# Performance work log

Hardware: AMD Instinct MI355X
Metric: run time of the kernel (lower is better)

Reference implementation:

```python
import jax, jax.numpy as jnp
import numpy as np

B, S, H, NH, DH, F, L = 4, 2048, 512, 8, 64, 2048, 4
ALPHA = 1.0   # config.lag_time_scale_alpha
EPS = 1e-12   # BERT layer_norm_eps
MS_PER_MIN = 60.0 * 1000.0


def setup_inputs() -> dict:
    key = jax.random.key(0)
    ks = jax.random.split(key, 24)
    p = lambda k, shape: (jax.random.normal(k, shape, jnp.float32) * 0.02)
    inp = {
        "query_states": jax.random.normal(ks[0], (B, S, H), jnp.float32),
        "attention_mask": jnp.zeros((B, 1, 1, S), jnp.float32),
        "position_bias": jax.random.normal(ks[1], (1, NH, S, S), jnp.float32) * 0.02,
        "timestamp": jnp.sort(jax.random.randint(ks[2], (B, S), 0, 36_000_000, jnp.int32), axis=-1),
        # stacked per-layer parameters (L leading dim)
        "wq": p(ks[3], (L, H, H)), "bq": jnp.zeros((L, H), jnp.float32),
        "wk": p(ks[4], (L, H, H)), "bk": jnp.zeros((L, H), jnp.float32),
        "wv": p(ks[5], (L, H, H)), "bv": jnp.zeros((L, H), jnp.float32),
        "wo": p(ks[6], (L, H, H)), "bo": jnp.zeros((L, H), jnp.float32),
        "ln1_g": jnp.ones((L, H), jnp.float32), "ln1_b": jnp.zeros((L, H), jnp.float32),
        "wi": p(ks[7], (L, H, F)), "bi": jnp.zeros((L, F), jnp.float32),
        "wo2": p(ks[8], (L, F, H)), "bo2": jnp.zeros((L, H), jnp.float32),
        "ln2_g": jnp.ones((L, H), jnp.float32), "ln2_b": jnp.zeros((L, H), jnp.float32),
    }
    return inp


def _ln(x, g, b):
    m = x.mean(-1, keepdims=True)
    v = ((x - m) ** 2).mean(-1, keepdims=True)
    return (x - m) / jnp.sqrt(v + EPS) * g + b


def reference(query_states, attention_mask, position_bias, timestamp,
              wq, bq, wk, bk, wv, bv, wo, bo, ln1_g, ln1_b,
              wi, bi, wo2, bo2, ln2_g, ln2_b):
    # encoder (is_decoder=False) lag-time scale: (B,1,S,S)
    lag = (timestamp[:, None, :, None] - timestamp[:, None, None, :]).astype(jnp.float32) / MS_PER_MIN
    scale = np.sqrt(DH).astype(np.float32) - ALPHA / (jnp.clip(lag, 0.0) + 1.0) + ALPHA

    x = query_states
    for l in range(L):
        def proj(w, b):
            return (x @ w + b).reshape(B, S, NH, DH).transpose(0, 2, 1, 3)  # (B,NH,S,DH)
        q, k, v = proj(wq[l], bq[l]), proj(wk[l], bk[l]), proj(wv[l], bv[l])
        scores = jnp.einsum('bhqd,bhkd->bhqk', q, k) / scale + position_bias + attention_mask
        probs = jax.nn.softmax(scores, axis=-1)
        ctx = jnp.einsum('bhqk,bhkd->bhqd', probs, v).transpose(0, 2, 1, 3).reshape(B, S, H)
        attn = _ln(ctx @ wo[l] + bo[l] + x, ln1_g[l], ln1_b[l])
        ffn = jax.nn.gelu(attn @ wi[l] + bi[l], approximate=False) @ wo2[l] + bo2[l]
        x = _ln(ffn + attn, ln2_g[l], ln2_b[l])
    return x
```

## Files before the change

kernel.cpp:

```cpp
#include <hip/hip_runtime.h>
#include <stdint.h>

typedef unsigned short u16;
using half8   = __attribute__((ext_vector_type(8))) _Float16;
using half4v  = __attribute__((ext_vector_type(4))) _Float16;
using half2v  = __attribute__((ext_vector_type(2))) _Float16;
using float4v = __attribute__((ext_vector_type(4))) float;

#define L2E 1.4426950408889634f

__device__ inline float4v f4zero() { float4v z = {0.f, 0.f, 0.f, 0.f}; return z; }

__device__ inline u16 f2h(float f) {
  union { _Float16 h; u16 u; } v; v.h = (_Float16)f; return v.u;
}
__device__ inline float h2f(u16 u) {
  union { u16 u; _Float16 h; } v; v.u = u; return (float)v.h;
}

__device__ inline half2v cvtpk(float a, float b) {
  return __builtin_bit_cast(half2v, __builtin_amdgcn_cvt_pkrtz(a, b));
}
__device__ inline _Float16 hexp2_(_Float16 x) {
  _Float16 r;
  asm("v_exp_f16 %0, %1" : "=v"(r) : "v"(x));
  return r;
}
__device__ inline float fdot2f(half2v a, float c) {
#if __has_builtin(__builtin_amdgcn_fdot2)
  typedef __attribute__((ext_vector_type(2))) __fp16 h2r;
  return __builtin_amdgcn_fdot2(__builtin_bit_cast(h2r, a),
                                __builtin_bit_cast(h2r, 0x3C003C00u), c, false);
#else
  return c + (float)a.x + (float)a.y;
#endif
}

__device__ inline void glds16(const u16* g, u16* lds_base, int lane) {
#if __has_builtin(__builtin_amdgcn_global_load_lds)
  (void)lane;
  __builtin_amdgcn_global_load_lds((const __attribute__((address_space(1))) void*)g,
                                   (__attribute__((address_space(3))) void*)lds_base,
                                   16, 0, 0);
#else
  *(uint4*)(lds_base + (size_t)lane * 8) = *(const uint4*)g;
#endif
}

__global__ __launch_bounds__(256) void transpose_cast_kernel(
    const float* __restrict__ in, u16* __restrict__ out, int K, int N, size_t out_ls) {
  __shared__ float tile[32][33];
  const int tx = threadIdx.x & 31, ty = threadIdx.x >> 5;
  in  += (size_t)blockIdx.z * K * N;
  out += (size_t)blockIdx.z * out_ls;
  const int n  = blockIdx.x * 32 + tx;
  const int k0 = blockIdx.y * 32;
#pragma unroll
  for (int j = 0; j < 32; j += 8)
    tile[ty + j][tx] = in[(size_t)(k0 + ty + j) * N + n];
  __syncthreads();
  const int k = k0 + tx;
  const int n0 = blockIdx.x * 32;
#pragma unroll
  for (int j = 0; j < 32; j += 8)
    out[(size_t)(n0 + ty + j) * K + k] = f2h(tile[tx][ty + j]);
}

__global__ __launch_bounds__(256) void cast_kernel(const float* __restrict__ in,
                                                   u16* __restrict__ out) {
  const int i = (blockIdx.x * 256 + threadIdx.x) * 4;
  float4 t = *(const float4*)(in + i);
  ushort4 o;
  o.x = f2h(t.x); o.y = f2h(t.y); o.z = f2h(t.z); o.w = f2h(t.w);
  *(ushort4*)(out + i) = o;
}

__global__ __launch_bounds__(256) void pb_tile_kernel(const float* __restrict__ pb,
                                                      u16* __restrict__ pbT) {
  const int g  = blockIdx.x * 256 + threadIdx.x;
  const int mm = g & 15;
  const int q  = (g >> 4) & 2047;
  const int kbh = g >> 15;
  const int kb = kbh & 31, h = kbh >> 5;
  const float* src = pb + ((size_t)h * 2048 + q) * 2048 + kb * 64 + mm;
  ushort4 o;
  o.x = f2h(src[0]  * L2E);
  o.y = f2h(src[16] * L2E);
  o.z = f2h(src[32] * L2E);
  o.w = f2h(src[48] * L2E);
  *(ushort4*)(pbT + ((size_t)(h * 32 + kb) * 2048 + q) * 64 + mm * 4) = o;
}

__global__ __launch_bounds__(256) void inv_tile_kernel(const int* __restrict__ ts,
                                                       u16* __restrict__ invT) {
  const int g  = blockIdx.x * 256 + threadIdx.x;
  const int mm = g & 15;
  const int q  = (g >> 4) & 2047;
  const int kb = (g >> 15) & 31;
  const int b  = g >> 20;
  const int tq = ts[b * 2048 + q];
  ushort4 o;
  u16* op = (u16*)&o;
#pragma unroll
  for (int nb = 0; nb < 4; nb++) {
    const int k = kb * 64 + nb * 16 + mm;
    const int du = tq - ts[b * 2048 + k];
    const float u = (du > 0) ? (float)du : 0.f;
    op[nb] = f2h(fmaf(u, L2E, 86561.70245333781f) *
                 __builtin_amdgcn_rcpf(fmaf(u, 9.f, 480000.f)));
  }
  *(ushort4*)(invT + ((size_t)(b * 32 + kb) * 2048 + q) * 64 + mm * 4) = o;
}

__global__ __launch_bounds__(256) void maskts_kernel(const float* __restrict__ mask,
                                                     const int* __restrict__ ts,
                                                     float* __restrict__ maskE,
                                                     float* __restrict__ tsf) {
  const int i = blockIdx.x * 256 + threadIdx.x;
  maskE[i] = mask[i] * L2E;
  tsf[i]   = (float)ts[i];
}

template <int BM, int BN, int NN, int KK, int EPI>
__global__ __launch_bounds__(256) void gemm_kernel(
    const u16* __restrict__ A, const u16* __restrict__ Wt,
    const float* __restrict__ b0, const float* __restrict__ b1, const float* __restrict__ b2,
    const u16* __restrict__ resid,
    void* __restrict__ o0, void* __restrict__ o1, void* __restrict__ o2) {
  constexpr int FI = BM / 32;
  constexpr int FJB = BN / 32;
  constexpr int FIW = BM / 32;
  constexpr int FJW = BN / 32;
  constexpr int NT = KK / 64;
  __shared__ __align__(16) u16 smem[2 * BM * 64 + 2 * BN * 64];
  u16* As0 = smem;
  u16* Bs0 = smem + 2 * BM * 64;
  const int tid = threadIdx.x, lane = tid & 63, wv = tid >> 6;
  const int quad = lane >> 4, mm = lane & 15;
  const int m0 = blockIdx.x * BM, n0 = blockIdx.y * BN;
  const int wm = (wv >> 1) * (BM / 2), wn = (wv & 1) * (BN / 2);
  const int srow = tid >> 3, slot = tid & 7;
  const int chunk = slot ^ (srow & 7);
  const u16* Ag = A  + (size_t)(m0 + srow) * KK + chunk * 8;
  const u16* Bg = Wt + (size_t)(n0 + srow) * KK + chunk * 8;
  const int sw = mm & 7;

  float4v acc[FIW][FJW];
#pragma unroll
  for (int i = 0; i < FIW; i++)
#pragma unroll
    for (int j = 0; j < FJW; j++) acc[i][j] = f4zero();

#pragma unroll
  for (int i = 0; i < FI; i++)
    glds16(Ag + (size_t)i * 32 * KK, As0 + (size_t)(wv * 8 + i * 32) * 64, lane);
#pragma unroll
  for (int j = 0; j < FJB; j++)
    glds16(Bg + (size_t)j * 32 * KK, Bs0 + (size_t)(wv * 8 + j * 32) * 64, lane);

  int cur = 0;
#pragma unroll 2
  for (int kt = 0; kt < NT; kt++) {
    __syncthreads();

    if (kt + 1 < NT) {
      const size_t ko = (size_t)(kt + 1) * 64;
#pragma unroll
      for (int i = 0; i < FI; i++)
        glds16(Ag + (size_t)i * 32 * KK + ko,
               As0 + (size_t)(cur ^ 1) * BM * 64 + (size_t)(wv * 8 + i * 32) * 64, lane);
#pragma unroll
      for (int j = 0; j < FJB; j++)
        glds16(Bg + (size_t)j * 32 * KK + ko,
               Bs0 + (size_t)(cur ^ 1) * BN * 64 + (size_t)(wv * 8 + j * 32) * 64, lane);
    }

    const u16* Ac = As0 + (size_t)cur * BM * 64;
    const u16* Bc = Bs0 + (size_t)cur * BN * 64;
#pragma unroll
    for (int ks = 0; ks < 2; ks++) {
      half8 a[FIW], b[FJW];
#pragma unroll
      for (int i = 0; i < FIW; i++)
        a[i] = *(const half8*)(Ac + (size_t)(wm + i * 16 + mm) * 64 + (size_t)((ks * 4 + quad) ^ sw) * 8);
#pragma unroll
      for (int j = 0; j < FJW; j++)
        b[j] = *(const half8*)(Bc + (size_t)(wn + j * 16 + mm) * 64 + (size_t)((ks * 4 + quad) ^ sw) * 8);
#pragma unroll
      for (int i = 0; i < FIW; i++)
#pragma unroll
        for (int j = 0; j < FJW; j++)
          acc[i][j] = __builtin_amdgcn_mfma_f32_16x16x32_f16(a[i], b[j], acc[i][j], 0, 0, 0);
    }
    cur ^= 1;
  }

#pragma unroll
  for (int j = 0; j < FJW; j++) {
    const int gn = n0 + wn + j * 16 + mm;
    const float bias = b0[gn];
#pragma unroll
    for (int i = 0; i < FIW; i++)
#pragma unroll
      for (int r = 0; r < 4; r++) {
        const int gm = m0 + wm + i * 16 + quad * 4 + r;
        const float val = acc[i][j][r] + bias;
        const size_t idx = (size_t)gm * NN + gn;
        if (EPI == 2) {
          ((float*)o0)[idx] = val + h2f(resid[idx]);
        } else {
          const float z  = val * 0.70710678118654752f;
          const float az = fabsf(z);
          const float t  = __builtin_amdgcn_rcpf(1.0f + 0.3275911f * az);
          const float poly = t * (0.254829592f + t * (-0.284496736f +
                             t * (1.421413741f + t * (-1.453152027f + t * 1.061405429f))));
          const float e = __builtin_amdgcn_exp2f(-az * az * L2E);
          float erf_ = 1.0f - poly * e;
          erf_ = (z < 0.0f) ? -erf_ : erf_;
          ((u16*)o0)[idx] = f2h(val * 0.5f * (1.0f + erf_));
        }
      }
  }
  (void)b1; (void)b2; (void)o1; (void)o2;
}

template <int NN, int KK, int EPI>
__global__ __launch_bounds__(512) void gemm8_kernel(
    const u16* __restrict__ A, const u16* __restrict__ Wt,
    const float* __restrict__ b0, const float* __restrict__ b1, const float* __restrict__ b2,
    void* __restrict__ o0, void* __restrict__ o1, void* __restrict__ o2) {
  __shared__ __align__(16) u16 smem[256 * 64 + 128 * 64];
  u16* As = smem;
  u16* Bs = smem + 256 * 64;
  const int tid = threadIdx.x, lane = tid & 63, wv = tid >> 6;
  const int quad = lane >> 4, mm = lane & 15;
  const int m0 = blockIdx.x * 256, n0 = blockIdx.y * 128;
  const int wm = (wv >> 1) * 64, wn = (wv & 1) * 64;
  const int srow = tid >> 3, slot = tid & 7;
  const int chunk = slot ^ (srow & 7);
  const u16* Ag = A  + (size_t)(m0 + srow) * KK + chunk * 8;
  const u16* Bg = Wt + (size_t)(n0 + srow) * KK + chunk * 8;
  const int sw = mm & 7;

  float4v acc[4][4];
#pragma unroll
  for (int i = 0; i < 4; i++)
#pragma unroll
    for (int j = 0; j < 4; j++) acc[i][j] = f4zero();

  for (int kte = 0; kte < KK; kte += 64) {
#pragma unroll
    for (int p = 0; p < 4; p++)
      glds16(Ag + (size_t)(p * 64) * KK + kte, As + (size_t)(p * 64 + wv * 8) * 64, lane);
#pragma unroll
    for (int p = 0; p < 2; p++)
      glds16(Bg + (size_t)(p * 64) * KK + kte, Bs + (size_t)(p * 64 + wv * 8) * 64, lane);
    __syncthreads();

#pragma unroll
    for (int ks = 0; ks < 2; ks++) {
      half8 a[4], b[4];
#pragma unroll
      for (int i = 0; i < 4; i++)
        a[i] = *(const half8*)(As + (size_t)(wm + i * 16 + mm) * 64 + (size_t)((ks * 4 + quad) ^ sw) * 8);
#pragma unroll
      for (int j = 0; j < 4; j++)
        b[j] = *(const half8*)(Bs + (size_t)(wn + j * 16 + mm) * 64 + (size_t)((ks * 4 + quad) ^ sw) * 8);
#pragma unroll
      for (int i = 0; i < 4; i++)
#pragma unroll
        for (int j = 0; j < 4; j++)
          acc[i][j] = __builtin_amdgcn_mfma_f32_16x16x32_f16(a[i], b[j], acc[i][j], 0, 0, 0);
    }
    __syncthreads();
  }

  if constexpr (EPI == 4) {
    if (n0 >= 1024) {
      const int b_ = m0 >> 11, s_base = m0 & 2047;
      const int h0 = (n0 >> 6) & 7;
      u16* T = smem;
#pragma unroll
      for (int hp = 0; hp < 2; hp++) {
        __syncthreads();
        if ((wv >> 2) == hp) {
          const int lm = wm & 127;
#pragma unroll
          for (int j = 0; j < 4; j++) {
            const int cn = wn + j * 16 + mm;
            const float bias = b2[(n0 & 511) + cn];
#pragma unroll
            for (int i = 0; i < 4; i++)
#pragma unroll
              for (int r = 0; r < 4; r++)
                T[(lm + i * 16 + quad * 4 + r) * 130 + cn] = f2h(acc[i][j][r] + bias);
          }
        }
        __syncthreads();
        const int rr = tid >> 2, sq = tid & 3;
        const int hh = rr >> 6, dd = rr & 63;
        u16* outp = (u16*)o2 + ((size_t)((b_ * 8 + h0 + hh) * 64 + dd)) * 2048
                  + s_base + hp * 128 + sq * 32;
#pragma unroll
        for (int g = 0; g < 4; g++) {
          union { u16 u[8]; uint4 v; } pk;
#pragma unroll
          for (int e = 0; e < 8; e++) {
            const int sl = sq * 32 + g * 8 + e;
            const int tl = (sl & 64) + (((sl & 3) << 4) | ((sl & 63) >> 2));
            pk.u[e] = T[tl * 130 + rr];
          }
          *(uint4*)(outp + g * 8) = pk.v;
        }
      }
      return;
    }
#pragma unroll
    for (int j = 0; j < 4; j++) {
      const int gn = n0 + wn + j * 16 + mm;
      const int which = gn >> 9, col = gn & 511, h = (gn >> 6) & 7, d = gn & 63;
      const float* bp = (which == 0) ? b0 : b1;
      const float bias = bp[col];
      u16* dst = (which == 0) ? (u16*)o0 : (u16*)o1;
#pragma unroll
      for (int i = 0; i < 4; i++)
#pragma unroll
        for (int r = 0; r < 4; r++) {
          const int gm = m0 + wm + i * 16 + quad * 4 + r;
          const int b_ = gm >> 11, s_ = gm & 2047;
          dst[((size_t)((b_ * 8 + h) * 2048 + s_)) * 64 + d] = f2h(acc[i][j][r] + bias);
        }
    }
    return;
  }

#pragma unroll
  for (int j = 0; j < 4; j++) {
    const int gn = n0 + wn + j * 16 + mm;
    const float bias = b0[gn];
#pragma unroll
    for (int i = 0; i < 4; i++)
#pragma unroll
      for (int r = 0; r < 4; r++) {
        const int gm = m0 + wm + i * 16 + quad * 4 + r;
        const float val = acc[i][j][r] + bias;
        const size_t idx = (size_t)gm * NN + gn;
        const float z  = val * 0.70710678118654752f;
        const float az = fabsf(z);
        const float t  = __builtin_amdgcn_rcpf(1.0f + 0.3275911f * az);
        const float poly = t * (0.254829592f + t * (-0.284496736f +
                           t * (1.421413741f + t * (-1.453152027f + t * 1.061405429f))));
        const float e = __builtin_amdgcn_exp2f(-az * az * L2E);
        float erf_ = 1.0f - poly * e;
        erf_ = (z < 0.0f) ? -erf_ : erf_;
        ((u16*)o0)[idx] = f2h(val * 0.5f * (1.0f + erf_));
      }
  }
}

template <int TILED>
__global__ __launch_bounds__(512) void flash4_kernel(
    const u16* __restrict__ Q, const u16* __restrict__ Kb, const u16* __restrict__ Vt,
    const u16* __restrict__ pbT, const u16* __restrict__ invT,
    const float* __restrict__ pb32,
    const float* __restrict__ maskE, const float* __restrict__ tsf,
    u16* __restrict__ ctx) {
  __shared__ __align__(16) u16 Kls[2][64 * 64];
  __shared__ __align__(16) u16 Vls[2][64 * 64];
  __shared__ __align__(16) u16 P[8][16 * 64];
  const int tid = threadIdx.x, lane = tid & 63, w = tid >> 6;
  const int quad = lane >> 4, mm = lane & 15;
  const int bh = blockIdx.y, b_ = bh >> 3, h_ = bh & 7;
  const int q0 = blockIdx.x * 128 + w * 16;
  const size_t qk_base = (size_t)bh * 2048 * 64;
  const size_t v_base  = (size_t)bh * 64 * 2048;
  const int srow = lane >> 3, slot = lane & 7;
  const int chunk = slot ^ srow;
  const int sw = mm & 7;

  const u16* Kgl = Kb + qk_base + (size_t)(w * 8 + srow) * 64 + chunk * 8;
  const u16* Vgl = Vt + v_base + (size_t)(w * 8 + srow) * 2048 + chunk * 8;

  glds16(Kgl, &Kls[0][(w * 8) * 64], lane);
  glds16(Vgl, &Vls[0][(w * 8) * 64], lane);

  half8 aq[2];
#pragma unroll
  for (int t = 0; t < 2; t++)
    aq[t] = *(const half8*)(Q + qk_base + (size_t)(q0 + mm) * 64 + t * 32 + quad * 8);

  float tqf[4];
  if (TILED < 2) {
#pragma unroll
    for (int r = 0; r < 4; r++) tqf[r] = tsf[b_ * 2048 + q0 + quad * 4 + r];
  }

  float l_r[4] = {0.f, 0.f, 0.f, 0.f};
  float4v o[4];
#pragma unroll
  for (int ob = 0; ob < 4; ob++) o[ob] = f4zero();

  ushort4 pbc[4], invc[4]; float tkc[4], mkc[4];
  if (TILED >= 1) {
#pragma unroll
    for (int r = 0; r < 4; r++)
      pbc[r] = *(const ushort4*)(pbT + ((size_t)(h_ * 32) * 2048 + q0 + quad * 4 + r) * 64 + mm * 4);
  }
  if (TILED == 2) {
#pragma unroll
    for (int r = 0; r < 4; r++)
      invc[r] = *(const ushort4*)(invT + ((size_t)(b_ * 32) * 2048 + q0 + quad * 4 + r) * 64 + mm * 4);
  } else {
#pragma unroll
    for (int nb = 0; nb < 4; nb++) tkc[nb] = tsf[b_ * 2048 + nb * 16 + mm];
  }
#pragma unroll
  for (int nb = 0; nb < 4; nb++) mkc[nb] = maskE[b_ * 2048 + nb * 16 + mm];

  int cur = 0;
  for (int kt = 0; kt < 32; kt++) {
    const int k0 = kt * 64;
    __syncthreads();

    const int kn = (kt < 31) ? kt + 1 : kt;
    ushort4 pbn[4], invn[4]; float tkn[4], mkn[4];
    if (TILED >= 1) {
#pragma unroll
      for (int r = 0; r < 4; r++)
        pbn[r] = *(const ushort4*)(pbT + ((size_t)(h_ * 32 + kn) * 2048 + q0 + quad * 4 + r) * 64 + mm * 4);
    }
    if (TILED == 2) {
#pragma unroll
      for (int r = 0; r < 4; r++)
        invn[r] = *(const ushort4*)(invT + ((size_t)(b_ * 32 + kn) * 2048 + q0 + quad * 4 + r) * 64 + mm * 4);
    } else {
#pragma unroll
      for (int nb = 0; nb < 4; nb++) tkn[nb] = tsf[b_ * 2048 + kn * 64 + nb * 16 + mm];
    }
#pragma unroll
    for (int nb = 0; nb < 4; nb++) mkn[nb] = maskE[b_ * 2048 + kn * 64 + nb * 16 + mm];

    if (kt < 31) {
      const size_t ko = (size_t)(kt + 1) * 4096;
      const size_t vo = (size_t)(kt + 1) * 64;
      glds16(Kgl + ko, &Kls[cur ^ 1][(w * 8) * 64], lane);
      glds16(Vgl + vo, &Vls[cur ^ 1][(w * 8) * 64], lane);
    }

    const u16* Kc = Kls[cur];
    float4v s[4];
    __builtin_amdgcn_s_setprio(1);
#pragma unroll
    for (int nb = 0; nb < 4; nb++) {
      const half8 kf0 = *(const half8*)(Kc + (size_t)(nb * 16 + mm) * 64 + (size_t)(quad ^ sw) * 8);
      const half8 kf1 = *(const half8*)(Kc + (size_t)(nb * 16 + mm) * 64 + (size_t)((4 + quad) ^ sw) * 8);
      s[nb] = __builtin_amdgcn_mfma_f32_16x16x32_f16(aq[0], kf0, f4zero(), 0, 0, 0);
      s[nb] = __builtin_amdgcn_mfma_f32_16x16x32_f16(aq[1], kf1, s[nb], 0, 0, 0);
    }
    __builtin_amdgcn_s_setprio(0);

    const half2v mk01 = cvtpk(mkc[0], mkc[1]);
    const half2v mk23 = cvtpk(mkc[2], mkc[3]);
#pragma unroll
    for (int r = 0; r < 4; r++) {
      half2v pb01, pb23, iv01, iv23;
      if (TILED >= 1) {
        pb01 = *(const half2v*)&pbc[r].x;
        pb23 = *(const half2v*)&pbc[r].z;
      } else {
        float pv[4];
#pragma unroll
        for (int nb = 0; nb < 4; nb++)
          pv[nb] = pb32[((size_t)h_ * 2048 + q0 + quad * 4 + r) * 2048 + k0 + nb * 16 + mm] * L2E;
        pb01 = cvtpk(pv[0], pv[1]); pb23 = cvtpk(pv[2], pv[3]);
      }
      if (TILED == 2) {
        iv01 = *(const half2v*)&invc[r].x;
        iv23 = *(const half2v*)&invc[r].z;
      } else {
        float ivv[4];
#pragma unroll
        for (int nb = 0; nb < 4; nb++) {
          const float u = fmaxf(tqf[r] - tkc[nb], 0.f);
          ivv[nb] = fmaf(u, L2E, 86561.70245333781f) *
                    __builtin_amdgcn_rcpf(fmaf(u, 9.f, 480000.f));
        }
        iv01 = cvtpk(ivv[0], ivv[1]); iv23 = cvtpk(ivv[2], ivv[3]);
      }
      const half2v s01 = cvtpk(s[0][r], s[1][r]);
      const half2v s23 = cvtpk(s[2][r], s[3][r]);
      const half2v t01 = __builtin_elementwise_fma(s01, iv01, pb01 + mk01);
      const half2v t23 = __builtin_elementwise_fma(s23, iv23, pb23 + mk23);
      half2v p01, p23;
      p01.x = hexp2_(t01.x); p01.y = hexp2_(t01.y);
      p23.x = hexp2_(t23.x); p23.y = hexp2_(t23.y);
      l_r[r] = fdot2f(p01, l_r[r]);
      l_r[r] = fdot2f(p23, l_r[r]);
      const int prow = quad * 4 + r;
      union { half2v h2[2]; half4v h4; } uu;
      uu.h2[0] = p01; uu.h2[1] = p23;
      *(half4v*)((char*)P[w] + prow * 128 + ((mm * 8) ^ ((prow & 7) << 4))) = uu.h4;
    }

    const u16* Vc = Vls[cur];
    const char* Pb = (const char*)P[w] + mm * 128;
    const int pxor = (mm & 7) << 4;
    const half8 ap0 = *(const half8*)(Pb + ((quad * 16) ^ pxor));
    const half8 ap1 = *(const half8*)(Pb + ((64 + quad * 16) ^ pxor));
    __builtin_amdgcn_s_setprio(1);
#pragma unroll
    for (int ob = 0; ob < 4; ob++) {
      const half8 vf0 = *(const half8*)(Vc + (size_t)(ob * 16 + mm) * 64 + (size_t)(quad ^ sw) * 8);
      const half8 vf1 = *(const half8*)(Vc + (size_t)(ob * 16 + mm) * 64 + (size_t)((4 + quad) ^ sw) * 8);
      o[ob] = __builtin_amdgcn_mfma_f32_16x16x32_f16(ap0, vf0, o[ob], 0, 0, 0);
      o[ob] = __builtin_amdgcn_mfma_f32_16x16x32_f16(ap1, vf1, o[ob], 0, 0, 0);
    }
    __builtin_amdgcn_s_setprio(0);

#pragma unroll
    for (int r = 0; r < 4; r++) { pbc[r] = pbn[r]; invc[r] = invn[r]; }
#pragma unroll
    for (int nb = 0; nb < 4; nb++) { tkc[nb] = tkn[nb]; mkc[nb] = mkn[nb]; }
    cur ^= 1;
  }

#pragma unroll
  for (int r = 0; r < 4; r++) {
    float l = l_r[r];
#pragma unroll
    for (int sh = 1; sh < 16; sh <<= 1) l += __shfl_xor(l, sh, 64);
    const float rl = __builtin_amdgcn_rcpf(l);
    const int qrow = q0 + quad * 4 + r;
#pragma unroll
    for (int ob = 0; ob < 4; ob++)
      ctx[((size_t)b_ * 2048 + qrow) * 512 + h_ * 64 + ob * 16 + mm] = f2h(o[ob][r] * rl);
  }
}

__global__ __launch_bounds__(256) void ln_kernel(
    const float* __restrict__ in, const float* __restrict__ g, const float* __restrict__ bb,
    float* __restrict__ of, u16* __restrict__ obf) {
  const int lane = threadIdx.x & 63, w = threadIdx.x >> 6;
  const int row = blockIdx.x * 4 + w;
  const float* x = in + (size_t)row * 512;
  float v[8];
  const float4 t0 = *(const float4*)(x + lane * 8);
  const float4 t1 = *(const float4*)(x + lane * 8 + 4);
  v[0] = t0.x; v[1] = t0.y; v[2] = t0.z; v[3] = t0.w;
  v[4] = t1.x; v[5] = t1.y; v[6] = t1.z; v[7] = t1.w;
  float s = 0.f;
#pragma unroll
  for (int i = 0; i < 8; i++) s += v[i];
#pragma unroll
  for (int sh = 1; sh < 64; sh <<= 1) s += __shfl_xor(s, sh, 64);
  const float mean = s * (1.0f / 512.0f);
  float sq = 0.f;
#pragma unroll
  for (int i = 0; i < 8; i++) { const float d = v[i] - mean; sq += d * d; }
#pragma unroll
  for (int sh = 1; sh < 64; sh <<= 1) sq += __shfl_xor(sq, sh, 64);
  const float rstd = rsqrtf(sq * (1.0f / 512.0f) + 1e-12f);
#pragma unroll
  for (int i = 0; i < 8; i++) {
    const int col = lane * 8 + i;
    const float y = (v[i] - mean) * rstd * g[col] + bb[col];
    if (of) of[(size_t)row * 512 + col] = y;
    obf[(size_t)row * 512 + col] = f2h(y);
  }
}

extern "C" void kernel_launch(void* const* d_in, const int* in_sizes, int n_in,
                              void* d_out, int out_size, void* d_ws, size_t ws_size,
                              hipStream_t stream) {
  const float* x_in = (const float*)d_in[0];
  const float* mask = (const float*)d_in[1];
  const float* pb   = (const float*)d_in[2];
  const int*   ts   = (const int*)d_in[3];
  const float* wq = (const float*)d_in[4];  const float* bq = (const float*)d_in[5];
  const float* wk = (const float*)d_in[6];  const float* bk = (const float*)d_in[7];
  const float* wvp = (const float*)d_in[8]; const float* bv = (const float*)d_in[9];
  const float* wo = (const float*)d_in[10]; const float* bo = (const float*)d_in[11];
  const float* ln1g = (const float*)d_in[12]; const float* ln1b = (const float*)d_in[13];
  const float* wi = (const float*)d_in[14]; const float* bi = (const float*)d_in[15];
  const float* wo2 = (const float*)d_in[16]; const float* bo2 = (const float*)d_in[17];
  const float* ln2g = (const float*)d_in[18]; const float* ln2b = (const float*)d_in[19];

  char* ws = (char*)d_ws;
  const size_t o_wqkv  = 0;
  const size_t o_woT   = 6291456;
  const size_t o_wiT   = 8388608;
  const size_t o_wo2T  = 16777216;
  const size_t o_maskE = 25165824;
  const size_t o_tsf   = 25198592;
  const size_t o_xbf   = 25231360;
  const size_t o_qb    = 33619968;
  const size_t o_kb    = 42008576;
  const size_t o_vb    = 50397184;
  const size_t o_ctx   = 58785792;
  const size_t o_attnb = 67174400;
  const size_t o_tmp   = 75563008;
  const size_t o_pbT   = 92340224;
  const size_t o_invT  = 159449088;
  const int tiled = (ws_size >= o_invT + 33554432ull) ? 2
                  : (ws_size >= o_pbT + 67108864ull) ? 1 : 0;

  u16*   wqkvT = (u16*)(ws + o_wqkv);
  u16*   woT   = (u16*)(ws + o_woT);
  u16*   wiT   = (u16*)(ws + o_wiT);
  u16*   wo2T  = (u16*)(ws + o_wo2T);
  float* maskE = (float*)(ws + o_maskE);
  float* tsf   = (float*)(ws + o_tsf);
  u16*   xbf   = (u16*)(ws + o_xbf);
  u16*   qb    = (u16*)(ws + o_qb);
  u16*   kb    = (u16*)(ws + o_kb);
  u16*   vb    = (u16*)(ws + o_vb);
  u16*   ctx   = (u16*)(ws + o_ctx);
  u16*   hb    = (u16*)(ws + o_qb);
  u16*   attnb = (u16*)(ws + o_attnb);
  float* tmp   = (float*)(ws + o_tmp);
  u16*   pbT   = (u16*)(ws + o_pbT);
  u16*   invT  = (u16*)(ws + o_invT);

  const dim3 blk(256);
  const dim3 blk512(512);
  transpose_cast_kernel<<<dim3(16, 16, 4), blk, 0, stream>>>(wq,  wqkvT,          512, 512, 786432);
  transpose_cast_kernel<<<dim3(16, 16, 4), blk, 0, stream>>>(wk,  wqkvT + 262144, 512, 512, 786432);
  transpose_cast_kernel<<<dim3(16, 16, 4), blk, 0, stream>>>(wvp, wqkvT + 524288, 512, 512, 786432);
  transpose_cast_kernel<<<dim3(16, 16, 4), blk, 0, stream>>>(wo,  woT,  512, 512,  262144);
  transpose_cast_kernel<<<dim3(64, 16, 4), blk, 0, stream>>>(wi,  wiT,  512, 2048, 1048576);
  transpose_cast_kernel<<<dim3(16, 64, 4), blk, 0, stream>>>(wo2, wo2T, 2048, 512, 1048576);
  maskts_kernel<<<32, blk, 0, stream>>>(mask, ts, maskE, tsf);
  cast_kernel<<<4096, blk, 0, stream>>>(x_in, xbf);
  if (tiled >= 1) pb_tile_kernel<<<32768, blk, 0, stream>>>(pb, pbT);
  if (tiled == 2) inv_tile_kernel<<<16384, blk, 0, stream>>>(ts, invT);

  for (int l = 0; l < 4; l++) {
    gemm8_kernel<1536, 512, 4><<<dim3(32, 12), blk512, 0, stream>>>(
        xbf, wqkvT + (size_t)l * 786432, bq + l * 512, bk + l * 512, bv + l * 512,
        qb, kb, vb);
    if (tiled == 2)
      flash4_kernel<2><<<dim3(16, 32), blk512, 0, stream>>>(qb, kb, vb, pbT, invT, pb, maskE, tsf, ctx);
    else if (tiled == 1)
      flash4_kernel<1><<<dim3(16, 32), blk512, 0, stream>>>(qb, kb, vb, pbT, nullptr, pb, maskE, tsf, ctx);
    else
      flash4_kernel<0><<<dim3(16, 32), blk512, 0, stream>>>(qb, kb, vb, nullptr, nullptr, pb, maskE, tsf, ctx);
    gemm_kernel<128, 64, 512, 512, 2><<<dim3(64, 8), blk, 0, stream>>>(
        ctx, woT + (size_t)l * 262144, bo + l * 512, nullptr, nullptr, xbf,
        tmp, nullptr, nullptr);
    ln_kernel<<<2048, blk, 0, stream>>>(tmp, ln1g + l * 512, ln1b + l * 512, nullptr, attnb);
    gemm8_kernel<2048, 512, 3><<<dim3(32, 16), blk512, 0, stream>>>(
        attnb, wiT + (size_t)l * 1048576, bi + l * 2048, nullptr, nullptr,
        hb, nullptr, nullptr);
    gemm_kernel<128, 64, 512, 2048, 2><<<dim3(64, 8), blk, 0, stream>>>(
        hb, wo2T + (size_t)l * 1048576, bo2 + l * 512, nullptr, nullptr, attnb,
        tmp, nullptr, nullptr);
    ln_kernel<<<2048, blk, 0, stream>>>(tmp, ln2g + l * 512, ln2b + l * 512,
                                        (l == 3) ? (float*)d_out : nullptr, xbf);
  }
  (void)in_sizes; (void)n_in; (void)out_size;
}
```

Measured before the change: 1.123 ms.

## Replace attention loop syncthreads with partial vmcnt wait and move next-tile bias loads

The attention kernel's per-iteration __syncthreads is replaced by an explicit s_waitcnt vmcnt(N) plus s_barrier, fenced with sched_barriers. The intent is that only the older async K/V LDS loads must finish, while the prefetched bias, mask and timestamp loads stay in flight. Those next-tile loads now go straight into the current registers after the P writes, not into separate pbn/invn buffers, which lowers register pressure. The hand-counted vmcnt values depend on the exact number and order of outstanding memory ops, so a miscount could cause a race or extra stalls. The sched barriers also limit how freely the compiler can interleave instructions.

Result: no change. 1.127 ms (+0.4%).

```diff
diff --git a/kernel.cpp b/kernel.cpp
--- a/kernel.cpp
+++ b/kernel.cpp
@@ -383,6 +383,7 @@
 
   glds16(Kgl, &Kls[0][(w * 8) * 64], lane);
   glds16(Vgl, &Vls[0][(w * 8) * 64], lane);
+  __builtin_amdgcn_sched_barrier(0);
 
   half8 aq[2];
 #pragma unroll
@@ -420,32 +421,16 @@
   int cur = 0;
   for (int kt = 0; kt < 32; kt++) {
     const int k0 = kt * 64;
-    __syncthreads();
-
-    const int kn = (kt < 31) ? kt + 1 : kt;
-    ushort4 pbn[4], invn[4]; float tkn[4], mkn[4];
-    if (TILED >= 1) {
-#pragma unroll
-      for (int r = 0; r < 4; r++)
-        pbn[r] = *(const ushort4*)(pbT + ((size_t)(h_ * 32 + kn) * 2048 + q0 + quad * 4 + r) * 64 + mm * 4);
-    }
-    if (TILED == 2) {
-#pragma unroll
-      for (int r = 0; r < 4; r++)
-        invn[r] = *(const ushort4*)(invT + ((size_t)(b_ * 32 + kn) * 2048 + q0 + quad * 4 + r) * 64 + mm * 4);
-    } else {
-#pragma unroll
-      for (int nb = 0; nb < 4; nb++) tkn[nb] = tsf[b_ * 2048 + kn * 64 + nb * 16 + mm];
-    }
-#pragma unroll
-    for (int nb = 0; nb < 4; nb++) mkn[nb] = maskE[b_ * 2048 + kn * 64 + nb * 16 + mm];
+    if constexpr (TILED == 0) asm volatile("s_waitcnt vmcnt(8)" ::: "memory");
+    else                      asm volatile("s_waitcnt vmcnt(12)" ::: "memory");
+    __builtin_amdgcn_s_barrier();
+    __builtin_amdgcn_sched_barrier(0);
 
     if (kt < 31) {
-      const size_t ko = (size_t)(kt + 1) * 4096;
-      const size_t vo = (size_t)(kt + 1) * 64;
-      glds16(Kgl + ko, &Kls[cur ^ 1][(w * 8) * 64], lane);
-      glds16(Vgl + vo, &Vls[cur ^ 1][(w * 8) * 64], lane);
-    }
+      glds16(Kgl + (size_t)(kt + 1) * 4096, &Kls[cur ^ 1][(w * 8) * 64], lane);
+      glds16(Vgl + (size_t)(kt + 1) * 64,   &Vls[cur ^ 1][(w * 8) * 64], lane);
+    }
+    __builtin_amdgcn_sched_barrier(0);
 
     const u16* Kc = Kls[cur];
     float4v s[4];
@@ -502,6 +487,25 @@
       *(half4v*)((char*)P[w] + prow * 128 + ((mm * 8) ^ ((prow & 7) << 4))) = uu.h4;
     }
 
+    if (kt < 31) {
+      const int kn = kt + 1;
+      if (TILED >= 1) {
+#pragma unroll
+        for (int r = 0; r < 4; r++)
+          pbc[r] = *(const ushort4*)(pbT + ((size_t)(h_ * 32 + kn) * 2048 + q0 + quad * 4 + r) * 64 + mm * 4);
+      }
+      if (TILED == 2) {
+#pragma unroll
+        for (int r = 0; r < 4; r++)
+          invc[r] = *(const ushort4*)(invT + ((size_t)(b_ * 32 + kn) * 2048 + q0 + quad * 4 + r) * 64 + mm * 4);
+      } else {
+#pragma unroll
+        for (int nb = 0; nb < 4; nb++) tkc[nb] = tsf[b_ * 2048 + kn * 64 + nb * 16 + mm];
+      }
+#pragma unroll
+      for (int nb = 0; nb < 4; nb++) mkc[nb] = maskE[b_ * 2048 + kn * 64 + nb * 16 + mm];
+    }
+
     const u16* Vc = Vls[cur];
     const char* Pb = (const char*)P[w] + mm * 128;
     const int pxor = (mm & 7) << 4;
@@ -516,11 +520,6 @@
       o[ob] = __builtin_amdgcn_mfma_f32_16x16x32_f16(ap1, vf1, o[ob], 0, 0, 0);
     }
     __builtin_amdgcn_s_setprio(0);
-
-#pragma unroll
-    for (int r = 0; r < 4; r++) { pbc[r] = pbn[r]; invc[r] = invn[r]; }
-#pragma unroll
-    for (int nb = 0; nb < 4; nb++) { tkc[nb] = tkn[nb]; mkc[nb] = mkn[nb]; }
     cur ^= 1;
   }
 
```
